# Optimization experiments

Measured on AMD Instinct MI355X. Metric: run time of the kernel, lower is better.

## Reference

```python
import jax, jax.numpy as jnp
import numpy as np

N_NODE = 50000
N_EDGE = 800000
D = 64       # in_dim = out_dim = hidden_dim
A = 64       # attn_dim
N_REL = 475  # 2*237+1 relation ids
B = 32       # batch of queries


def setup_inputs() -> dict:
    key = jax.random.key(0)
    ks = jax.random.split(key, 16)
    hidden = jax.random.normal(ks[0], (N_NODE, D), dtype=jnp.float32)
    sub = jax.random.randint(ks[1], (N_EDGE,), 0, N_NODE)
    rel = jax.random.randint(ks[2], (N_EDGE,), 0, N_REL)
    obj = jax.random.randint(ks[3], (N_EDGE,), 0, N_NODE)
    edges = jnp.stack([sub, rel, obj], axis=1)  # [E, 3]
    gnn_emb_rel = jax.random.normal(ks[4], (N_REL, D), dtype=jnp.float32)
    mapping = jax.random.randint(ks[5], (N_REL,), 0, N_REL)  # rel id -> unique-rel row
    q_rel = jax.random.randint(ks[6], (B,), 0, N_REL)
    r_idx = jax.random.randint(ks[7], (N_EDGE,), 0, B)  # edge -> query index
    s = 1.0 / np.sqrt(D)
    sa = 1.0 / np.sqrt(A)
    u = lambda k, shape, b: jax.random.uniform(k, shape, jnp.float32, minval=-b, maxval=b)
    return {
        "hidden": hidden,
        "edges": edges,
        "gnn_emb_rel": gnn_emb_rel,
        "mapping": mapping,
        "q_rel": q_rel,
        "r_idx": r_idx,
        "n_node": N_NODE,
        "Ws_w": u(ks[8], (A, D), s),
        "Wr_w": u(ks[9], (A, D), s),
        "Wqr_w": u(ks[10], (A, D), s),
        "Wqr_b": u(ks[11], (A,), s),
        "walpha_w": u(ks[12], (1, A), sa),
        "walpha_b": u(ks[13], (1,), sa),
        "Wh_w": u(ks[14], (D, D), s),
    }


def reference(hidden, edges, gnn_emb_rel, mapping, q_rel, r_idx, n_node,
              Ws_w, Wr_w, Wqr_w, Wqr_b, walpha_w, walpha_b, Wh_w):
    sub, rel, obj = edges[:, 0], edges[:, 1], edges[:, 2]
    hs = hidden[sub]                       # [E, D] gather
    hr = gnn_emb_rel[mapping[rel]]         # [E, D] gather
    # per-query h_qr projected once, then gathered per edge (same math, cheaper)
    hq = gnn_emb_rel[mapping[q_rel]]       # [B, D]
    qr_attn = hq @ Wqr_w.T + Wqr_b         # [B, A]
    pre = hs @ Ws_w.T + hr @ Wr_w.T + qr_attn[r_idx]   # [E, A]
    alpha = jax.nn.sigmoid(jax.nn.relu(pre) @ walpha_w.T + walpha_b)  # [E, 1]
    message = alpha * (hs * hr)            # [E, D]
    message_agg = jax.ops.segment_sum(message, obj, num_segments=n_node)  # [N, D]
    hidden_new = jax.nn.relu(message_agg @ Wh_w.T)  # act = ReLU from GNN_auto
    return hidden_new
```

## Files before the change

### kernel.cpp

```cpp
#include <hip/hip_runtime.h>
#include <hip/hip_bf16.h>

#define D64 64
#define WTP 65
#define LPAD 68

typedef __attribute__((ext_vector_type(8))) short short8;
typedef __attribute__((ext_vector_type(4))) float f32x4;

__device__ inline float lane_bcast(float v, int l) {
    return __uint_as_float(__builtin_amdgcn_readlane(__float_as_uint(v), l));
}
__device__ inline float bf16_lo(unsigned u) { return __uint_as_float(u << 16); }
__device__ inline float bf16_hi(unsigned u) { return __uint_as_float(u & 0xFFFF0000u); }
__device__ inline float bf16u(unsigned short u) { return __uint_as_float((unsigned)u << 16); }
__device__ inline unsigned short f2bf(float f) {
    __hip_bfloat16 b = __float2bfloat16(f);
    return *(unsigned short*)&b;
}

__global__ void prep_kernel(const float* __restrict__ emb, const int* __restrict__ mapping,
                            const int* __restrict__ q_rel,
                            const float* __restrict__ Wr, const float* __restrict__ Wqr,
                            const float* __restrict__ Wqr_b, const float* __restrict__ Ws,
                            unsigned short* __restrict__ hrmapb,
                            unsigned short* __restrict__ hrWb,
                            unsigned short* __restrict__ qrb,
                            unsigned short* __restrict__ WsB, int nrel, int nq) {
    int b = blockIdx.x;
    int lane = threadIdx.x;
    if (b < nrel) {
        int m = mapping[b];
        float v = emb[m * D64 + lane];
        hrmapb[b * D64 + lane] = f2bf(v);
        float acc = 0.f;
#pragma unroll
        for (int d = 0; d < D64; ++d)
            acc = fmaf(lane_bcast(v, d), Wr[lane * D64 + d], acc);
        hrWb[b * D64 + lane] = f2bf(acc);
    } else if (b < nrel + nq) {
        int q = b - nrel;
        int m = mapping[q_rel[q]];
        float v = emb[m * D64 + lane];
        float acc = Wqr_b[lane];
#pragma unroll
        for (int d = 0; d < D64; ++d)
            acc = fmaf(lane_bcast(v, d), Wqr[lane * D64 + d], acc);
        qrb[q * D64 + lane] = f2bf(acc);
    } else {
        int c = b - nrel - nq;
        WsB[c * D64 + lane] = f2bf(Ws[c * D64 + lane]);
    }
}

__global__ void rowmm_mfma_kernel(const float* __restrict__ in,
                                  const unsigned short* __restrict__ WsB,
                                  unsigned short* __restrict__ outb,
                                  unsigned short* __restrict__ inb, int nrows) {
    __shared__ unsigned short la[16 * LPAD];
    int lane = threadIdx.x;
    int rbase = blockIdx.x * 16;
    if (rbase >= nrows) return;

    short8 bfrag[8];
#pragma unroll
    for (int t = 0; t < 4; ++t)
#pragma unroll
        for (int kk = 0; kk < 2; ++kk)
            bfrag[t * 2 + kk] = *(const short8*)(WsB + (size_t)(t * 16 + (lane & 15)) * D64 +
                                                 kk * 32 + (lane >> 4) * 8);

#pragma unroll
    for (int rr = 0; rr < 16; ++rr) {
        int r = rbase + rr;
        float v = (r < nrows) ? in[(size_t)r * D64 + lane] : 0.f;
        unsigned short bb = f2bf(v);
        if (r < nrows) inb[(size_t)r * D64 + lane] = bb;
        la[rr * LPAD + lane] = bb;
    }

    f32x4 acc[4];
#pragma unroll
    for (int t = 0; t < 4; ++t) acc[t] = (f32x4){0.f, 0.f, 0.f, 0.f};
#pragma unroll
    for (int kk = 0; kk < 2; ++kk) {
        short8 afrag = *(const short8*)(la + (lane & 15) * LPAD + kk * 32 + (lane >> 4) * 8);
#pragma unroll
        for (int t = 0; t < 4; ++t)
            acc[t] = __builtin_amdgcn_mfma_f32_16x16x32_bf16(afrag, bfrag[t * 2 + kk],
                                                             acc[t], 0, 0, 0);
    }
#pragma unroll
    for (int t = 0; t < 4; ++t)
#pragma unroll
        for (int reg = 0; reg < 4; ++reg) {
            int row = rbase + (lane >> 4) * 4 + reg;
            int col = t * 16 + (lane & 15);
            if (row < nrows)
                outb[(size_t)row * D64 + col] = f2bf(acc[t][reg]);
        }
}

__global__ void hist_pack_kernel(const int* __restrict__ edges, const int* __restrict__ r_idx,
                                 int* __restrict__ counts, uint2* __restrict__ epack, int E) {
    int i4 = blockIdx.x * blockDim.x + threadIdx.x;
    int n4 = E >> 2;
    if (i4 < n4) {
        const uint4* e4 = (const uint4*)edges;
        uint4 a = e4[i4 * 3 + 0];
        uint4 b = e4[i4 * 3 + 1];
        uint4 c = e4[i4 * 3 + 2];
        uint4 r = ((const uint4*)r_idx)[i4];
        uint4 p01 = make_uint4(a.x | (a.y << 17) | (r.x << 26), a.z,
                               a.w | (b.x << 17) | (r.y << 26), b.y);
        uint4 p23 = make_uint4(b.z | (b.w << 17) | (r.z << 26), c.x,
                               c.y | (c.z << 17) | (r.w << 26), c.w);
        ((uint4*)epack)[i4 * 2 + 0] = p01;
        ((uint4*)epack)[i4 * 2 + 1] = p23;
        atomicAdd(&counts[a.z], 1);
        atomicAdd(&counts[b.y], 1);
        atomicAdd(&counts[c.x], 1);
        atomicAdd(&counts[c.w], 1);
    }
    int tail = n4 * 4;
    int ti = tail + i4;
    if (i4 < (E - tail) && ti < E) {
        int sub = edges[ti * 3 + 0];
        int rel = edges[ti * 3 + 1];
        int obj = edges[ti * 3 + 2];
        int ri  = r_idx[ti];
        epack[ti] = make_uint2((unsigned)sub | ((unsigned)rel << 17) | ((unsigned)ri << 26),
                               (unsigned)obj);
        atomicAdd(&counts[obj], 1);
    }
}

__global__ void scan1_kernel(const int* __restrict__ counts, int* __restrict__ offs,
                             int* __restrict__ partials, int n) {
    __shared__ int tsum[256];
    int t = threadIdx.x;
    int base = blockIdx.x * 1024 + t * 4;
    int v[4];
    int s = 0;
#pragma unroll
    for (int i = 0; i < 4; ++i) {
        int idx = base + i;
        int c = (idx < n) ? counts[idx] : 0;
        v[i] = s;
        s += c;
    }
    tsum[t] = s;
    __syncthreads();
    for (int off = 1; off < 256; off <<= 1) {
        int y = (t >= off) ? tsum[t - off] : 0;
        __syncthreads();
        tsum[t] += y;
        __syncthreads();
    }
    int incl = tsum[t];
    int thread_prefix = incl - s;
    if (t == 255) partials[blockIdx.x] = incl;
#pragma unroll
    for (int i = 0; i < 4; ++i) {
        int idx = base + i;
        if (idx < n) offs[idx] = thread_prefix + v[i];
    }
}

__global__ void scan2_kernel(int* partials, int nb) {
    int t = threadIdx.x;
    int own = (t < nb) ? partials[t] : 0;
    int v = own;
    for (int off = 1; off < 64; off <<= 1) {
        int y = __shfl_up(v, off, 64);
        if (t >= off) v += y;
    }
    if (t < nb) partials[t] = v - own;
}

__global__ void scan3_kernel(int* __restrict__ offs, const int* __restrict__ partials, int n) {
    int base = blockIdx.x * 1024 + threadIdx.x;
    int add = partials[blockIdx.x];
#pragma unroll
    for (int i = 0; i < 4; ++i) {
        int idx = base + i * 256;
        if (idx < n) offs[idx] += add;
    }
}

__global__ void alpha_scatter_kernel(const uint2* __restrict__ epack,
                                     const unsigned short* __restrict__ hsWb,
                                     const unsigned short* __restrict__ hrWb,
                                     const unsigned short* __restrict__ qrb,
                                     const float* __restrict__ walpha_w,
                                     const float* __restrict__ walpha_b,
                                     int* __restrict__ offs, int2* __restrict__ rec,
                                     int E, int half) {
    int tid = blockIdx.x * blockDim.x + threadIdx.x;
    int e0 = tid >> 3;
    int l = tid & 7;
    if (e0 >= half) return;
    int e1 = e0 + half;
    bool has1 = (e1 < E);

    uint2 p0 = epack[e0];
    uint2 p1 = has1 ? epack[e1] : make_uint2(0u, 0u);
    int sub0 = p0.x & 0x1FFFF, rel0 = (p0.x >> 17) & 0x1FF, ri0 = p0.x >> 26, obj0 = (int)p0.y;
    int sub1 = p1.x & 0x1FFFF, rel1 = (p1.x >> 17) & 0x1FF, ri1 = p1.x >> 26, obj1 = (int)p1.y;

    uint4 hv0 = *(const uint4*)(hsWb + (size_t)sub0 * D64 + l * 8);
    uint4 rv0 = *(const uint4*)(hrWb + (size_t)rel0 * D64 + l * 8);
    uint4 qv0 = *(const uint4*)(qrb  + (size_t)ri0  * D64 + l * 8);
    uint4 hv1 = *(const uint4*)(hsWb + (size_t)sub1 * D64 + l * 8);
    uint4 rv1 = *(const uint4*)(hrWb + (size_t)rel1 * D64 + l * 8);
    uint4 qv1 = *(const uint4*)(qrb  + (size_t)ri1  * D64 + l * 8);
    const float4* w = (const float4*)(walpha_w + l * 8);
    float4 w0 = w[0], w1 = w[1];

    float x0, x1;
    x0 = fmaxf(bf16_lo(hv0.x) + bf16_lo(rv0.x) + bf16_lo(qv0.x), 0.f) * w0.x;
    x0 = fmaf(fmaxf(bf16_hi(hv0.x) + bf16_hi(rv0.x) + bf16_hi(qv0.x), 0.f), w0.y, x0);
    x0 = fmaf(fmaxf(bf16_lo(hv0.y) + bf16_lo(rv0.y) + bf16_lo(qv0.y), 0.f), w0.z, x0);
    x0 = fmaf(fmaxf(bf16_hi(hv0.y) + bf16_hi(rv0.y) + bf16_hi(qv0.y), 0.f), w0.w, x0);
    x0 = fmaf(fmaxf(bf16_lo(hv0.z) + bf16_lo(rv0.z) + bf16_lo(qv0.z), 0.f), w1.x, x0);
    x0 = fmaf(fmaxf(bf16_hi(hv0.z) + bf16_hi(rv0.z) + bf16_hi(qv0.z), 0.f), w1.y, x0);
    x0 = fmaf(fmaxf(bf16_lo(hv0.w) + bf16_lo(rv0.w) + bf16_lo(qv0.w), 0.f), w1.z, x0);
    x0 = fmaf(fmaxf(bf16_hi(hv0.w) + bf16_hi(rv0.w) + bf16_hi(qv0.w), 0.f), w1.w, x0);

    x1 = fmaxf(bf16_lo(hv1.x) + bf16_lo(rv1.x) + bf16_lo(qv1.x), 0.f) * w0.x;
    x1 = fmaf(fmaxf(bf16_hi(hv1.x) + bf16_hi(rv1.x) + bf16_hi(qv1.x), 0.f), w0.y, x1);
    x1 = fmaf(fmaxf(bf16_lo(hv1.y) + bf16_lo(rv1.y) + bf16_lo(qv1.y), 0.f), w0.z, x1);
    x1 = fmaf(fmaxf(bf16_hi(hv1.y) + bf16_hi(rv1.y) + bf16_hi(qv1.y), 0.f), w0.w, x1);
    x1 = fmaf(fmaxf(bf16_lo(hv1.z) + bf16_lo(rv1.z) + bf16_lo(qv1.z), 0.f), w1.x, x1);
    x1 = fmaf(fmaxf(bf16_hi(hv1.z) + bf16_hi(rv1.z) + bf16_hi(qv1.z), 0.f), w1.y, x1);
    x1 = fmaf(fmaxf(bf16_lo(hv1.w) + bf16_lo(rv1.w) + bf16_lo(qv1.w), 0.f), w1.z, x1);
    x1 = fmaf(fmaxf(bf16_hi(hv1.w) + bf16_hi(rv1.w) + bf16_hi(qv1.w), 0.f), w1.w, x1);

    x0 += __shfl_xor(x0, 4, 64);
    x1 += __shfl_xor(x1, 4, 64);
    x0 += __shfl_xor(x0, 2, 64);
    x1 += __shfl_xor(x1, 2, 64);
    x0 += __shfl_xor(x0, 1, 64);
    x1 += __shfl_xor(x1, 1, 64);

    if (l == 0) {
        float wb = walpha_b[0];
        float a0 = 1.f / (1.f + __expf(-(x0 + wb)));
        int slot0 = atomicAdd(&offs[obj0], 1);
        rec[slot0] = make_int2(sub0 | (rel0 << 17), __float_as_int(a0));
        if (has1) {
            float a1 = 1.f / (1.f + __expf(-(x1 + wb)));
            int slot1 = atomicAdd(&offs[obj1], 1);
            rec[slot1] = make_int2(sub1 | (rel1 << 17), __float_as_int(a1));
        }
    }
}

__global__ void agg_wh_kernel(const int2* __restrict__ rec, const int* __restrict__ endoff,
                              const unsigned short* __restrict__ hiddenb,
                              const unsigned short* __restrict__ hrmapb,
                              const float* __restrict__ Wh,
                              float* __restrict__ out, int NN) {
    __shared__ float WT[D64 * WTP];
    int tid = threadIdx.x;
    for (int i = tid; i < D64 * D64; i += blockDim.x)
        WT[(i & 63) * WTP + (i >> 6)] = Wh[i];
    __syncthreads();
    int lane = tid & 63;
    int n = (blockIdx.x * blockDim.x + tid) >> 6;
    if (n >= NN) return;
    int start = (n == 0) ? 0 : endoff[n - 1];
    int end = endoff[n];
    start = __builtin_amdgcn_readfirstlane(start);
    end = __builtin_amdgcn_readfirstlane(end);
    float acc0 = 0.f, acc1 = 0.f, acc2 = 0.f, acc3 = 0.f;
    for (int base = start; base < end; base += 64) {
        int cnt = end - base;
        if (cnt > 64) cnt = 64;
        int rx = 0, ry = 0;
        if (lane < cnt) {
            int2 r = rec[base + lane];
            rx = r.x; ry = r.y;
        }
        int j = 0;
        for (; j + 7 < cnt; j += 8) {
            int a_rx[8], a_ry[8];
#pragma unroll
            for (int k = 0; k < 8; ++k) {
                a_rx[k] = __builtin_amdgcn_readlane(rx, j + k);
                a_ry[k] = __builtin_amdgcn_readlane(ry, j + k);
            }
            float h[8], m[8];
#pragma unroll
            for (int k = 0; k < 8; ++k) {
                h[k] = bf16u(hiddenb[(size_t)(a_rx[k] & 0x1FFFF) * D64 + lane]);
                m[k] = bf16u(hrmapb[(size_t)((unsigned)a_rx[k] >> 17) * D64 + lane]);
            }
            acc0 = fmaf(__uint_as_float(a_ry[0]) * h[0], m[0], acc0);
            acc1 = fmaf(__uint_as_float(a_ry[1]) * h[1], m[1], acc1);
            acc2 = fmaf(__uint_as_float(a_ry[2]) * h[2], m[2], acc2);
            acc3 = fmaf(__uint_as_float(a_ry[3]) * h[3], m[3], acc3);
            acc0 = fmaf(__uint_as_float(a_ry[4]) * h[4], m[4], acc0);
            acc1 = fmaf(__uint_as_float(a_ry[5]) * h[5], m[5], acc1);
            acc2 = fmaf(__uint_as_float(a_ry[6]) * h[6], m[6], acc2);
            acc3 = fmaf(__uint_as_float(a_ry[7]) * h[7], m[7], acc3);
        }
        for (; j + 3 < cnt; j += 4) {
            int rx0 = __builtin_amdgcn_readlane(rx, j);
            int ry0 = __builtin_amdgcn_readlane(ry, j);
            int rx1 = __builtin_amdgcn_readlane(rx, j + 1);
            int ry1 = __builtin_amdgcn_readlane(ry, j + 1);
            int rx2 = __builtin_amdgcn_readlane(rx, j + 2);
            int ry2 = __builtin_amdgcn_readlane(ry, j + 2);
            int rx3 = __builtin_amdgcn_readlane(rx, j + 3);
            int ry3 = __builtin_amdgcn_readlane(ry, j + 3);
            float h0 = bf16u(hiddenb[(size_t)(rx0 & 0x1FFFF) * D64 + lane]);
            float m0 = bf16u(hrmapb[(size_t)((unsigned)rx0 >> 17) * D64 + lane]);
            float h1 = bf16u(hiddenb[(size_t)(rx1 & 0x1FFFF) * D64 + lane]);
            float m1 = bf16u(hrmapb[(size_t)((unsigned)rx1 >> 17) * D64 + lane]);
            float h2 = bf16u(hiddenb[(size_t)(rx2 & 0x1FFFF) * D64 + lane]);
            float m2 = bf16u(hrmapb[(size_t)((unsigned)rx2 >> 17) * D64 + lane]);
            float h3 = bf16u(hiddenb[(size_t)(rx3 & 0x1FFFF) * D64 + lane]);
            float m3 = bf16u(hrmapb[(size_t)((unsigned)rx3 >> 17) * D64 + lane]);
            acc0 = fmaf(__uint_as_float(ry0) * h0, m0, acc0);
            acc1 = fmaf(__uint_as_float(ry1) * h1, m1, acc1);
            acc2 = fmaf(__uint_as_float(ry2) * h2, m2, acc2);
            acc3 = fmaf(__uint_as_float(ry3) * h3, m3, acc3);
        }
        for (; j < cnt; ++j) {
            int rx0 = __builtin_amdgcn_readlane(rx, j);
            int ry0 = __builtin_amdgcn_readlane(ry, j);
            float h0 = bf16u(hiddenb[(size_t)(rx0 & 0x1FFFF) * D64 + lane]);
            float m0 = bf16u(hrmapb[(size_t)((unsigned)rx0 >> 17) * D64 + lane]);
            acc0 = fmaf(__uint_as_float(ry0) * h0, m0, acc0);
        }
    }
    float acc = (acc0 + acc1) + (acc2 + acc3);
    float o = 0.f;
#pragma unroll
    for (int d = 0; d < D64; ++d)
        o = fmaf(lane_bcast(acc, d), WT[d * WTP + lane], o);
    out[(size_t)n * D64 + lane] = fmaxf(o, 0.f);
}

extern "C" void kernel_launch(void* const* d_in, const int* in_sizes, int n_in,
                              void* d_out, int out_size, void* d_ws, size_t ws_size,
                              hipStream_t stream) {
    const float* hidden   = (const float*)d_in[0];
    const int*   edges    = (const int*)d_in[1];
    const float* emb_rel  = (const float*)d_in[2];
    const int*   mapping  = (const int*)d_in[3];
    const int*   q_rel    = (const int*)d_in[4];
    const int*   r_idx    = (const int*)d_in[5];
    const float* Ws_w     = (const float*)d_in[7];
    const float* Wr_w     = (const float*)d_in[8];
    const float* Wqr_w    = (const float*)d_in[9];
    const float* Wqr_b    = (const float*)d_in[10];
    const float* walpha_w = (const float*)d_in[11];
    const float* walpha_b = (const float*)d_in[12];
    const float* Wh_w     = (const float*)d_in[13];
    float* out = (float*)d_out;

    int NN   = in_sizes[0] / D64;
    int E    = in_sizes[5];
    int NREL = in_sizes[3];
    int NQ   = in_sizes[4];

    char* ws = (char*)d_ws;
    size_t off = 0;
    unsigned short* hsWb    = (unsigned short*)(ws + off); off += (size_t)NN * D64 * 2;
    unsigned short* hiddenb = (unsigned short*)(ws + off); off += (size_t)NN * D64 * 2;
    int2*  rec  = (int2*)(ws + off);       off += (size_t)E * sizeof(int2);
    uint2* epack = (uint2*)(ws + off);     off += (size_t)E * sizeof(uint2);
    int* counts = (int*)(ws + off);        off += (size_t)NN * sizeof(int);
    int* offs   = (int*)(ws + off);        off += (size_t)NN * sizeof(int);
    int* partials = (int*)(ws + off);      off += 64 * sizeof(int);
    unsigned short* hrmapb = (unsigned short*)(ws + off); off += (size_t)NREL * D64 * 2;
    unsigned short* hrWb   = (unsigned short*)(ws + off); off += (size_t)NREL * D64 * 2;
    unsigned short* qrb    = (unsigned short*)(ws + off); off += (size_t)NQ * D64 * 2;
    unsigned short* WsB    = (unsigned short*)(ws + off); off += (size_t)D64 * D64 * 2;

    int NB = (NN + 1023) / 1024;

    hipMemsetAsync(counts, 0, (size_t)NN * sizeof(int), stream);
    prep_kernel<<<NREL + NQ + 64, 64, 0, stream>>>(emb_rel, mapping, q_rel, Wr_w, Wqr_w,
                                                   Wqr_b, Ws_w, hrmapb, hrWb, qrb, WsB,
                                                   NREL, NQ);
    rowmm_mfma_kernel<<<(NN + 15) / 16, 64, 0, stream>>>(hidden, WsB, hsWb, hiddenb, NN);
    {
        int n4 = (E + 3) / 4;
        hist_pack_kernel<<<(n4 + 255) / 256, 256, 0, stream>>>(edges, r_idx, counts, epack, E);
    }
    scan1_kernel<<<NB, 256, 0, stream>>>(counts, offs, partials, NN);
    scan2_kernel<<<1, 64, 0, stream>>>(partials, NB);
    scan3_kernel<<<NB, 256, 0, stream>>>(offs, partials, NN);
    {
        int half = (E + 1) / 2;
        long long threads = (long long)half * 8;
        int blocks = (int)((threads + 255) / 256);
        alpha_scatter_kernel<<<blocks, 256, 0, stream>>>(epack, hsWb, hrWb, qrb,
                                                         walpha_w, walpha_b, offs, rec, E, half);
    }
    agg_wh_kernel<<<(NN * 64 + 1023) / 1024, 1024, 0, stream>>>(rec, offs, hiddenb, hrmapb,
                                                                Wh_w, out, NN);
}
```

Measured before the change: 155.6 us.

## Precombine relation and query projections into a table indexed per edge

A new comb_kernel precomputes hrW[r]+qr[q] for every (relation, query) pair into a bf16 table of NREL*32 rows. The edge pack now stores a combined index rel*32+ri, so alpha_scatter does two row gathers per edge instead of three and fewer adds. The counts memset is also folded into prep_kernel as extra zeroing blocks, removing a separate memset call. The cost is an extra kernel launch, a table of roughly 1.9 MB, and one more bf16 rounding step on the combined sum.

```diff
diff --git a/kernel.cpp b/kernel.cpp
--- a/kernel.cpp
+++ b/kernel.cpp
@@ -26,7 +26,8 @@
                             unsigned short* __restrict__ hrmapb,
                             unsigned short* __restrict__ hrWb,
                             unsigned short* __restrict__ qrb,
-                            unsigned short* __restrict__ WsB, int nrel, int nq) {
+                            unsigned short* __restrict__ WsB,
+                            int* __restrict__ counts, int nrel, int nq, int NN) {
     int b = blockIdx.x;
     int lane = threadIdx.x;
     if (b < nrel) {
@@ -47,9 +48,27 @@
         for (int d = 0; d < D64; ++d)
             acc = fmaf(lane_bcast(v, d), Wqr[lane * D64 + d], acc);
         qrb[q * D64 + lane] = f2bf(acc);
-    } else {
+    } else if (b < nrel + nq + 64) {
         int c = b - nrel - nq;
         WsB[c * D64 + lane] = f2bf(Ws[c * D64 + lane]);
+    } else {
+        int c = b - nrel - nq - 64;
+        int idx = c * 64 + lane;
+        if (idx < NN) counts[idx] = 0;
+    }
+}
+
+__global__ void comb_kernel(const unsigned short* __restrict__ hrWb,
+                            const unsigned short* __restrict__ qrb,
+                            unsigned short* __restrict__ combb, int nrel) {
+    int i = blockIdx.x * blockDim.x + threadIdx.x;
+    int total = nrel * 32 * D64;
+    if (i < total) {
+        int lane = i & 63;
+        int row = i >> 6;
+        int r = row >> 5;
+        int q = row & 31;
+        combb[i] = f2bf(bf16u(hrWb[r * D64 + lane]) + bf16u(qrb[q * D64 + lane]));
     }
 }
 
@@ -111,10 +130,10 @@
         uint4 b = e4[i4 * 3 + 1];
         uint4 c = e4[i4 * 3 + 2];
         uint4 r = ((const uint4*)r_idx)[i4];
-        uint4 p01 = make_uint4(a.x | (a.y << 17) | (r.x << 26), a.z,
-                               a.w | (b.x << 17) | (r.y << 26), b.y);
-        uint4 p23 = make_uint4(b.z | (b.w << 17) | (r.z << 26), c.x,
-                               c.y | (c.z << 17) | (r.w << 26), c.w);
+        uint4 p01 = make_uint4(a.x | ((((a.y << 5) | r.x)) << 17), a.z,
+                               a.w | ((((b.x << 5) | r.y)) << 17), b.y);
+        uint4 p23 = make_uint4(b.z | ((((b.w << 5) | r.z)) << 17), c.x,
+                               c.y | ((((c.z << 5) | r.w)) << 17), c.w);
         ((uint4*)epack)[i4 * 2 + 0] = p01;
         ((uint4*)epack)[i4 * 2 + 1] = p23;
         atomicAdd(&counts[a.z], 1);
@@ -125,12 +144,11 @@
     int tail = n4 * 4;
     int ti = tail + i4;
     if (i4 < (E - tail) && ti < E) {
-        int sub = edges[ti * 3 + 0];
-        int rel = edges[ti * 3 + 1];
-        int obj = edges[ti * 3 + 2];
-        int ri  = r_idx[ti];
-        epack[ti] = make_uint2((unsigned)sub | ((unsigned)rel << 17) | ((unsigned)ri << 26),
-                               (unsigned)obj);
+        unsigned sub = edges[ti * 3 + 0];
+        unsigned rel = edges[ti * 3 + 1];
+        unsigned obj = edges[ti * 3 + 2];
+        unsigned ri  = r_idx[ti];
+        epack[ti] = make_uint2(sub | (((rel << 5) | ri) << 17), obj);
         atomicAdd(&counts[obj], 1);
     }
 }
@@ -190,8 +208,7 @@
 
 __global__ void alpha_scatter_kernel(const uint2* __restrict__ epack,
                                      const unsigned short* __restrict__ hsWb,
-                                     const unsigned short* __restrict__ hrWb,
-                                     const unsigned short* __restrict__ qrb,
+                                     const unsigned short* __restrict__ combb,
                                      const float* __restrict__ walpha_w,
                                      const float* __restrict__ walpha_b,
                                      int* __restrict__ offs, int2* __restrict__ rec,
@@ -205,36 +222,35 @@
 
     uint2 p0 = epack[e0];
     uint2 p1 = has1 ? epack[e1] : make_uint2(0u, 0u);
-    int sub0 = p0.x & 0x1FFFF, rel0 = (p0.x >> 17) & 0x1FF, ri0 = p0.x >> 26, obj0 = (int)p0.y;
-    int sub1 = p1.x & 0x1FFFF, rel1 = (p1.x >> 17) & 0x1FF, ri1 = p1.x >> 26, obj1 = (int)p1.y;
-
-    uint4 hv0 = *(const uint4*)(hsWb + (size_t)sub0 * D64 + l * 8);
-    uint4 rv0 = *(const uint4*)(hrWb + (size_t)rel0 * D64 + l * 8);
-    uint4 qv0 = *(const uint4*)(qrb  + (size_t)ri0  * D64 + l * 8);
-    uint4 hv1 = *(const uint4*)(hsWb + (size_t)sub1 * D64 + l * 8);
-    uint4 rv1 = *(const uint4*)(hrWb + (size_t)rel1 * D64 + l * 8);
-    uint4 qv1 = *(const uint4*)(qrb  + (size_t)ri1  * D64 + l * 8);
+    unsigned sub0 = p0.x & 0x1FFFF, comb0 = p0.x >> 17;
+    unsigned sub1 = p1.x & 0x1FFFF, comb1 = p1.x >> 17;
+    int obj0 = (int)p0.y, obj1 = (int)p1.y;
+
+    uint4 hv0 = *(const uint4*)(hsWb  + (size_t)sub0  * D64 + l * 8);
+    uint4 cv0 = *(const uint4*)(combb + (size_t)comb0 * D64 + l * 8);
+    uint4 hv1 = *(const uint4*)(hsWb  + (size_t)sub1  * D64 + l * 8);
+    uint4 cv1 = *(const uint4*)(combb + (size_t)comb1 * D64 + l * 8);
     const float4* w = (const float4*)(walpha_w + l * 8);
     float4 w0 = w[0], w1 = w[1];
 
     float x0, x1;
-    x0 = fmaxf(bf16_lo(hv0.x) + bf16_lo(rv0.x) + bf16_lo(qv0.x), 0.f) * w0.x;
-    x0 = fmaf(fmaxf(bf16_hi(hv0.x) + bf16_hi(rv0.x) + bf16_hi(qv0.x), 0.f), w0.y, x0);
-    x0 = fmaf(fmaxf(bf16_lo(hv0.y) + bf16_lo(rv0.y) + bf16_lo(qv0.y), 0.f), w0.z, x0);
-    x0 = fmaf(fmaxf(bf16_hi(hv0.y) + bf16_hi(rv0.y) + bf16_hi(qv0.y), 0.f), w0.w, x0);
-    x0 = fmaf(fmaxf(bf16_lo(hv0.z) + bf16_lo(rv0.z) + bf16_lo(qv0.z), 0.f), w1.x, x0);
-    x0 = fmaf(fmaxf(bf16_hi(hv0.z) + bf16_hi(rv0.z) + bf16_hi(qv0.z), 0.f), w1.y, x0);
-    x0 = fmaf(fmaxf(bf16_lo(hv0.w) + bf16_lo(rv0.w) + bf16_lo(qv0.w), 0.f), w1.z, x0);
-    x0 = fmaf(fmaxf(bf16_hi(hv0.w) + bf16_hi(rv0.w) + bf16_hi(qv0.w), 0.f), w1.w, x0);
-
-    x1 = fmaxf(bf16_lo(hv1.x) + bf16_lo(rv1.x) + bf16_lo(qv1.x), 0.f) * w0.x;
-    x1 = fmaf(fmaxf(bf16_hi(hv1.x) + bf16_hi(rv1.x) + bf16_hi(qv1.x), 0.f), w0.y, x1);
-    x1 = fmaf(fmaxf(bf16_lo(hv1.y) + bf16_lo(rv1.y) + bf16_lo(qv1.y), 0.f), w0.z, x1);
-    x1 = fmaf(fmaxf(bf16_hi(hv1.y) + bf16_hi(rv1.y) + bf16_hi(qv1.y), 0.f), w0.w, x1);
-    x1 = fmaf(fmaxf(bf16_lo(hv1.z) + bf16_lo(rv1.z) + bf16_lo(qv1.z), 0.f), w1.x, x1);
-    x1 = fmaf(fmaxf(bf16_hi(hv1.z) + bf16_hi(rv1.z) + bf16_hi(qv1.z), 0.f), w1.y, x1);
-    x1 = fmaf(fmaxf(bf16_lo(hv1.w) + bf16_lo(rv1.w) + bf16_lo(qv1.w), 0.f), w1.z, x1);
-    x1 = fmaf(fmaxf(bf16_hi(hv1.w) + bf16_hi(rv1.w) + bf16_hi(qv1.w), 0.f), w1.w, x1);
+    x0 = fmaxf(bf16_lo(hv0.x) + bf16_lo(cv0.x), 0.f) * w0.x;
+    x0 = fmaf(fmaxf(bf16_hi(hv0.x) + bf16_hi(cv0.x), 0.f), w0.y, x0);
+    x0 = fmaf(fmaxf(bf16_lo(hv0.y) + bf16_lo(cv0.y), 0.f), w0.z, x0);
+    x0 = fmaf(fmaxf(bf16_hi(hv0.y) + bf16_hi(cv0.y), 0.f), w0.w, x0);
+    x0 = fmaf(fmaxf(bf16_lo(hv0.z) + bf16_lo(cv0.z), 0.f), w1.x, x0);
+    x0 = fmaf(fmaxf(bf16_hi(hv0.z) + bf16_hi(cv0.z), 0.f), w1.y, x0);
+    x0 = fmaf(fmaxf(bf16_lo(hv0.w) + bf16_lo(cv0.w), 0.f), w1.z, x0);
+    x0 = fmaf(fmaxf(bf16_hi(hv0.w) + bf16_hi(cv0.w), 0.f), w1.w, x0);
+
+    x1 = fmaxf(bf16_lo(hv1.x) + bf16_lo(cv1.x), 0.f) * w0.x;
+    x1 = fmaf(fmaxf(bf16_hi(hv1.x) + bf16_hi(cv1.x), 0.f), w0.y, x1);
+    x1 = fmaf(fmaxf(bf16_lo(hv1.y) + bf16_lo(cv1.y), 0.f), w0.z, x1);
+    x1 = fmaf(fmaxf(bf16_hi(hv1.y) + bf16_hi(cv1.y), 0.f), w0.w, x1);
+    x1 = fmaf(fmaxf(bf16_lo(hv1.z) + bf16_lo(cv1.z), 0.f), w1.x, x1);
+    x1 = fmaf(fmaxf(bf16_hi(hv1.z) + bf16_hi(cv1.z), 0.f), w1.y, x1);
+    x1 = fmaf(fmaxf(bf16_lo(hv1.w) + bf16_lo(cv1.w), 0.f), w1.z, x1);
+    x1 = fmaf(fmaxf(bf16_hi(hv1.w) + bf16_hi(cv1.w), 0.f), w1.w, x1);
 
     x0 += __shfl_xor(x0, 4, 64);
     x1 += __shfl_xor(x1, 4, 64);
@@ -246,12 +262,14 @@
     if (l == 0) {
         float wb = walpha_b[0];
         float a0 = 1.f / (1.f + __expf(-(x0 + wb)));
+        int rel0 = comb0 >> 5;
         int slot0 = atomicAdd(&offs[obj0], 1);
-        rec[slot0] = make_int2(sub0 | (rel0 << 17), __float_as_int(a0));
+        rec[slot0] = make_int2((int)(sub0 | (rel0 << 17)), __float_as_int(a0));
         if (has1) {
             float a1 = 1.f / (1.f + __expf(-(x1 + wb)));
+            int rel1 = comb1 >> 5;
             int slot1 = atomicAdd(&offs[obj1], 1);
-            rec[slot1] = make_int2(sub1 | (rel1 << 17), __float_as_int(a1));
+            rec[slot1] = make_int2((int)(sub1 | (rel1 << 17)), __float_as_int(a1));
         }
     }
 }
@@ -379,13 +397,17 @@
     unsigned short* hrWb   = (unsigned short*)(ws + off); off += (size_t)NREL * D64 * 2;
     unsigned short* qrb    = (unsigned short*)(ws + off); off += (size_t)NQ * D64 * 2;
     unsigned short* WsB    = (unsigned short*)(ws + off); off += (size_t)D64 * D64 * 2;
+    unsigned short* combb  = (unsigned short*)(ws + off); off += (size_t)NREL * 32 * D64 * 2;
 
     int NB = (NN + 1023) / 1024;
 
-    hipMemsetAsync(counts, 0, (size_t)NN * sizeof(int), stream);
-    prep_kernel<<<NREL + NQ + 64, 64, 0, stream>>>(emb_rel, mapping, q_rel, Wr_w, Wqr_w,
-                                                   Wqr_b, Ws_w, hrmapb, hrWb, qrb, WsB,
-                                                   NREL, NQ);
+    {
+        int zblocks = (NN + 63) / 64;
+        prep_kernel<<<NREL + NQ + 64 + zblocks, 64, 0, stream>>>(
+            emb_rel, mapping, q_rel, Wr_w, Wqr_w, Wqr_b, Ws_w,
+            hrmapb, hrWb, qrb, WsB, counts, NREL, NQ, NN);
+    }
+    comb_kernel<<<(NREL * 32 * D64 + 255) / 256, 256, 0, stream>>>(hrWb, qrb, combb, NREL);
     rowmm_mfma_kernel<<<(NN + 15) / 16, 64, 0, stream>>>(hidden, WsB, hsWb, hiddenb, NN);
     {
         int n4 = (E + 3) / 4;
@@ -398,7 +420,7 @@
         int half = (E + 1) / 2;
         long long threads = (long long)half * 8;
         int blocks = (int)((threads + 255) / 256);
-        alpha_scatter_kernel<<<blocks, 256, 0, stream>>>(epack, hsWb, hrWb, qrb,
+        alpha_scatter_kernel<<<blocks, 256, 0, stream>>>(epack, hsWb, combb,
                                                          walpha_w, walpha_b, offs, rec, E, half);
     }
     agg_wh_kernel<<<(NN * 64 + 1023) / 1024, 1024, 0, stream>>>(rec, offs, hiddenb, hrmapb,
```

Measured after the change: 156.7 us. About the same (+0.7%).
